# Kernel tuning notes

Hardware: AMD Instinct MI355X
Metric: run time of the kernel (lower is better)

## Reference

```python
import jax, jax.numpy as jnp
import numpy as np

B, BS, M, D = 64, 8, 512, 256  # b = bs * neg_sample_num, neg_sample_num = 8
NEG_FILL = -1e10


def setup_inputs() -> dict:
    key = jax.random.key(0)
    ks = jax.random.split(key, 7)
    x = jax.random.normal(ks[0], (B, M, D), jnp.float32)
    y = jax.random.normal(ks[1], (BS, M, D), jnp.float32)
    mask_x = jax.random.randint(ks[2], (B, M), 0, 2).astype(bool).at[:, 0].set(True)
    mask_y = jax.random.randint(ks[3], (BS, M), 0, 2).astype(bool).at[:, 0].set(True)
    scale = 1.0 / np.sqrt(D)
    Wq = jax.random.normal(ks[4], (D, D), jnp.float32) * scale  # torch Linear weight [out,in]
    Wk = jax.random.normal(ks[5], (D, D), jnp.float32) * scale
    Wv = jax.random.normal(ks[6], (D, D), jnp.float32) * scale
    return {"x": x, "y": y, "mask_x": mask_x, "mask_y": mask_y, "Wq": Wq, "Wk": Wk, "Wv": Wv}


def reference(x, y, mask_x, mask_y, Wq, Wk, Wv):
    # Projections (torch Linear: x @ W.T, no bias)
    Qx, Kx, Vx = x @ Wq.T, x @ Wk.T, x @ Wv.T
    Qy, Ky, Vy = y @ Wq.T, y @ Wk.T, y @ Wv.T
    b, m, d = Qx.shape
    bs = Ky.shape[0]
    neg = b // bs  # neg_sample_num branch (bs != b)

    scores_x = jnp.einsum('bid,bjd->bij', Qx, Kx)   # [b,m,m]
    scores_y = jnp.einsum('bid,bjd->bij', Qy, Ky)   # [bs,m,m]
    # Q_x grouped as [bs, neg, m, d] then transposed to [neg, bs, m, d];
    # K_y is tiled over neg (pure broadcast), so contract directly against [bs,m,d].
    Qx_e = Qx.reshape(bs, neg, m, d).swapaxes(0, 1)  # [neg,bs,m,d]
    scores_xy = jnp.einsum('nsid,sjd->nsij', Qx_e, Ky)  # [neg,bs,m,m]

    mx = mask_x[:, :, None]  # [b,m,1]
    my = mask_y[:, :, None]  # [bs,m,1]
    scores_x = jnp.where(mx & mx.swapaxes(1, 2), scores_x, NEG_FILL)
    scores_y = jnp.where(my & my.swapaxes(1, 2), scores_y, NEG_FILL)

    mask_xy = mask_x.reshape(bs, neg, m, 1).swapaxes(0, 1) & mask_y[None, :, None, :]  # [neg,bs,m,m]
    scores_xy = jnp.where(mask_xy, scores_xy, NEG_FILL)

    # y_len[n, s] = sum(mask_y[s]) for every n (repeat/view/sum/transpose in torch)
    y_len = jnp.broadcast_to(jnp.sum(mask_y.astype(jnp.int32), axis=1)[None, :], (neg, bs))

    probs_x = jax.nn.softmax(scores_x, axis=-1)
    probs_y = jax.nn.softmax(scores_y, axis=-1)
    probs_xy = jax.nn.softmax(scores_xy, axis=-1)

    ctx_x = jnp.einsum('bij,bjd->bid', probs_x, Vx)
    ctx_y = jnp.einsum('bij,bjd->bid', probs_y, Vy)
    return (ctx_x, ctx_y, scores_x, scores_y, probs_xy, mask_xy, y_len)
```

## Files before the change

### kernel.cpp

```cpp
#include <hip/hip_runtime.h>
#include <cstdint>

#define NEG_FILL_F (-10000000000.0f)
constexpr int BB     = 64;
constexpr int BS_    = 8;
constexpr int MM     = 512;
constexpr int DD     = 256;
constexpr int ROWS_X = BB * MM;
constexpr int ROWS_Y = BS_ * MM;
constexpr int ROWS_ALL = ROWS_X + ROWS_Y;
constexpr int KS     = 512;

typedef __attribute__((ext_vector_type(8))) short short8;
typedef __attribute__((ext_vector_type(4))) float f32x4;

__device__ inline unsigned short rne_bf16(float f) {
    unsigned int u = __float_as_uint(f);
    u = (u + 0x7FFFu + ((u >> 16) & 1u)) >> 16;
    return (unsigned short)u;
}
__device__ inline float bf2f(unsigned short h) {
    return __uint_as_float(((unsigned int)h) << 16);
}

__device__ inline f32x4 mfma16(short8 a, short8 b, f32x4 c) {
    return __builtin_amdgcn_mfma_f32_16x16x32_bf16(a, b, c, 0, 0, 0);
}

__device__ inline void gld16(const unsigned short* g, unsigned short* l) {
    __builtin_amdgcn_global_load_lds(
        (const __attribute__((address_space(1))) unsigned int*)g,
        (__attribute__((address_space(3))) unsigned int*)l, 16, 0, 0);
}

__device__ inline void mfma_4x4(const short8 af[4], const short8 bf_[4],
                                f32x4 acc[4][4]) {
    #pragma unroll
    for (int i = 0; i < 4; ++i)
        #pragma unroll
        for (int j = 0; j < 4; ++j)
            acc[i][j] = mfma16(af[i], bf_[j], acc[i][j]);
}

__device__ inline int awin(int w) { return ((((w >> 2) == 1) ? 256 : 0) + (w & 3) * 64); }
__device__ inline int bwin(int w) { return ((((w >> 2) == 2) ? 256 : 0) + (w & 3) * 64); }

__device__ inline void stage64(unsigned short* dstbase,
                               const unsigned short* __restrict__ src,
                               int srccol, int wave, int lane)
{
    #pragma unroll
    for (int s4 = 0; s4 < 4; ++s4) {
        const int c   = s4 * 256 + wave * 64 + lane;
        const int r   = c >> 3;
        const int cin = (c & 7) ^ (r & 7);
        gld16(src + (size_t)r * KS + srccol + cin * 8,
              dstbase + (size_t)(s4 * 256 + wave * 64) * 8);
    }
}

__device__ inline void frag4_x64(const unsigned short (*T)[64], int rbase,
                                 int lid, int c0, short8 f[4])
{
    const int q = c0 ^ (lid & 7);
    #pragma unroll
    for (int i = 0; i < 4; ++i)
        f[i] = *(const short8*)&T[rbase + i * 16 + lid][q * 8];
}

__global__ __launch_bounds__(256) void convw_kernel(
    const float* __restrict__ Wq, const float* __restrict__ Wk,
    const float* __restrict__ Wv, unsigned short* __restrict__ Wb)
{
    const int g  = blockIdx.x * 256 + threadIdx.x;
    const int e  = g * 8;
    const int zi = e >> 16;
    const int off = e & 65535;
    const int row = off >> 8, k0 = off & 255;
    const float* W = (zi == 0) ? Wq : (zi == 1 ? Wk : Wv);
    float4 v0 = *(const float4*)(W + off);
    float4 v1 = *(const float4*)(W + off + 4);
    const float fv[8] = {v0.x, v0.y, v0.z, v0.w, v1.x, v1.y, v1.z, v1.w};
    short8 hh, ll;
    #pragma unroll
    for (int i = 0; i < 8; ++i) {
        unsigned short h = rne_bf16(fv[i]);
        hh[i] = (short)h;
        ll[i] = (short)rne_bf16(fv[i] - bf2f(h));
    }
    unsigned short* dst = Wb + (size_t)zi * 131072 + (size_t)row * KS;
    *(short8*)(dst + k0)       = hh;
    *(short8*)(dst + 256 + k0) = ll;
}

__global__ __launch_bounds__(256) void convx_kernel(
    const float* __restrict__ x, const float* __restrict__ y,
    unsigned short* __restrict__ xs)
{
    const int g   = blockIdx.x * 256 + threadIdx.x;
    const int row = g >> 5;
    const int off = (g & 31) * 8;
    const float* src = (row < ROWS_X) ? (x + (size_t)row * DD)
                                      : (y + (size_t)(row - ROWS_X) * DD);
    float4 v0 = *(const float4*)(src + off);
    float4 v1 = *(const float4*)(src + off + 4);
    const float fv[8] = {v0.x, v0.y, v0.z, v0.w, v1.x, v1.y, v1.z, v1.w};
    short8 hh, ll;
    #pragma unroll
    for (int i = 0; i < 8; ++i) {
        unsigned short h = rne_bf16(fv[i]);
        hh[i] = (short)h;
        ll[i] = (short)rne_bf16(fv[i] - bf2f(h));
    }
    unsigned short* dst = xs + (size_t)row * KS;
    *(short8*)(dst + off)       = hh;
    *(short8*)(dst + 256 + off) = ll;
}

__global__ __launch_bounds__(256) void proj_kernel(
    const unsigned short* __restrict__ xs,
    const unsigned short* __restrict__ Wb,
    unsigned short* __restrict__ Qa, unsigned short* __restrict__ Kb,
    unsigned short* __restrict__ Vt)
{
    const int z    = blockIdx.z;
    const int row0 = blockIdx.x * 128;
    const int col0 = blockIdx.y * 128;
    const unsigned short* Asrc = xs + (size_t)row0 * KS;
    const unsigned short* Bsrc = Wb + (size_t)z * 131072 + (size_t)col0 * KS;

    __shared__ unsigned short Ab[128][64];
    __shared__ unsigned short Bb[128][64];

    const int t = threadIdx.x;
    const int wave = t >> 6, lane = t & 63, quad = lane >> 4, lid = lane & 15;
    const int wrow = (wave & 1) * 64, wcol = (wave >> 1) * 64;

    f32x4 acc[4][4];
    #pragma unroll
    for (int i = 0; i < 4; ++i)
        #pragma unroll
        for (int j = 0; j < 4; ++j) acc[i][j] = (f32x4){0.f, 0.f, 0.f, 0.f};

    for (int w = 0; w < 12; ++w) {
        stage64(&Ab[0][0], Asrc, awin(w), wave, lane);
        stage64(&Bb[0][0], Bsrc, bwin(w), wave, lane);
        __syncthreads();
        #pragma unroll
        for (int kk = 0; kk < 64; kk += 32) {
            const int c0 = (kk >> 3) + quad;
            short8 af[4], bf_[4];
            frag4_x64(Ab, wrow, lid, c0, af);
            frag4_x64(Bb, wcol, lid, c0, bf_);
            mfma_4x4(af, bf_, acc);
        }
        __syncthreads();
    }

    if (z == 2) {
        #pragma unroll
        for (int i = 0; i < 4; ++i) {
            const int rg = row0 + wrow + i * 16 + quad * 4;
            const int b  = rg >> 9;
            const int j  = rg & 511;
            #pragma unroll
            for (int jt = 0; jt < 4; ++jt) {
                const int col = col0 + wcol + jt * 16 + lid;
                *(ushort4*)(Vt + (size_t)b * DD * MM + (size_t)col * MM + j) =
                    make_ushort4(rne_bf16(acc[i][jt][0]), rne_bf16(acc[i][jt][1]),
                                 rne_bf16(acc[i][jt][2]), rne_bf16(acc[i][jt][3]));
            }
        }
    } else {
        unsigned short* dst = (z == 0) ? Qa : Kb;
        #pragma unroll
        for (int i = 0; i < 4; ++i) {
            const int rg = row0 + wrow + i * 16 + quad * 4;
            #pragma unroll
            for (int r = 0; r < 4; ++r) {
                unsigned short* rowp = dst + (size_t)(rg + r) * KS;
                #pragma unroll
                for (int jt = 0; jt < 4; ++jt) {
                    const int col = col0 + wcol + jt * 16 + lid;
                    const float v = acc[i][jt][r];
                    unsigned short h = rne_bf16(v);
                    rowp[col]       = h;
                    rowp[256 + col] = rne_bf16(v - bf2f(h));
                }
            }
        }
    }
}

__global__ __launch_bounds__(256) void scores_self_kernel(
    const unsigned short* __restrict__ Qa,
    const unsigned short* __restrict__ Kb,
    const int* __restrict__ mask_x, const int* __restrict__ mask_y,
    float* __restrict__ Sbase, float2* __restrict__ pstats)
{
    const int z    = blockIdx.z;
    const int row0 = blockIdx.x * 128;
    const int col0 = blockIdx.y * 128;
    const unsigned short* Asrc = Qa + (size_t)(z * MM + row0) * KS;
    const unsigned short* Bsrc = Kb + (size_t)(z * MM + col0) * KS;
    const int* msk = (z < 64) ? (mask_x + z * MM) : (mask_y + (z - 64) * MM);
    float* S = Sbase + (size_t)z * MM * MM;

    __shared__ unsigned short Ab[128][64];
    __shared__ unsigned short Bb[128][64];
    __shared__ float pm2[128][2];
    __shared__ float ps2[128][2];

    const int t = threadIdx.x;
    const int wave = t >> 6, lane = t & 63, quad = lane >> 4, lid = lane & 15;
    const int wrow = (wave & 1) * 64, wcol = (wave >> 1) * 64;

    f32x4 acc[4][4];
    #pragma unroll
    for (int i = 0; i < 4; ++i)
        #pragma unroll
        for (int j = 0; j < 4; ++j) acc[i][j] = (f32x4){0.f, 0.f, 0.f, 0.f};

    for (int w = 0; w < 12; ++w) {
        stage64(&Ab[0][0], Asrc, awin(w), wave, lane);
        stage64(&Bb[0][0], Bsrc, bwin(w), wave, lane);
        __syncthreads();
        #pragma unroll
        for (int kk = 0; kk < 64; kk += 32) {
            const int c0 = (kk >> 3) + quad;
            short8 af[4], bf_[4];
            frag4_x64(Ab, wrow, lid, c0, af);
            frag4_x64(Bb, wcol, lid, c0, bf_);
            mfma_4x4(af, bf_, acc);
        }
        __syncthreads();
    }

    int mcol[4];
    #pragma unroll
    for (int jt = 0; jt < 4; ++jt) mcol[jt] = msk[col0 + wcol + jt * 16 + lid];

    #pragma unroll
    for (int i = 0; i < 4; ++i) {
        const int rl0 = wrow + i * 16 + quad * 4;
        #pragma unroll
        for (int r = 0; r < 4; ++r) {
            const int rlocal = rl0 + r;
            const int rg = row0 + rlocal;
            const bool mr = (msk[rg] != 0);
            float* Srow = S + (size_t)rg * MM;
            float v[4];
            float mt = -3.4e38f;
            #pragma unroll
            for (int jt = 0; jt < 4; ++jt) {
                const int col = col0 + wcol + jt * 16 + lid;
                const bool valid = mr && (mcol[jt] != 0);
                v[jt] = valid ? acc[i][jt][r] : NEG_FILL_F;
                Srow[col] = v[jt];
                mt = fmaxf(mt, v[jt]);
            }
            #pragma unroll
            for (int o = 1; o < 16; o <<= 1) mt = fmaxf(mt, __shfl_xor(mt, o));
            float se = 0.f;
            #pragma unroll
            for (int jt = 0; jt < 4; ++jt) se += __expf(v[jt] - mt);
            #pragma unroll
            for (int o = 1; o < 16; o <<= 1) se += __shfl_xor(se, o);
            if (lid == 0) { pm2[rlocal][wave >> 1] = mt; ps2[rlocal][wave >> 1] = se; }
        }
    }
    __syncthreads();
    if (t < 128) {
        const float m0 = pm2[t][0], m1 = pm2[t][1];
        const float mm = fmaxf(m0, m1);
        const float ss = ps2[t][0] * __expf(m0 - mm) + ps2[t][1] * __expf(m1 - mm);
        pstats[(size_t)(z * 4 + blockIdx.y) * MM + row0 + t] = make_float2(mm, ss);
    }
}

__global__ __launch_bounds__(256) void scores_xy_kernel(
    const unsigned short* __restrict__ Qa, const unsigned short* __restrict__ Kb,
    const int* __restrict__ mask_x, const int* __restrict__ mask_y,
    float* __restrict__ Sbase, float* __restrict__ Mbase,
    float2* __restrict__ pstats)
{
    const int z = blockIdx.z;
    const int n = z >> 3, s = z & 7;
    const int bq = s * 8 + n;
    const int bk = s;
    const int row0 = blockIdx.x * 128;
    const int col0 = blockIdx.y * 128;
    const unsigned short* Asrc = Qa + (size_t)(bq * MM + row0) * KS;
    const unsigned short* Bsrc = Kb + (size_t)((ROWS_X + bk * MM) + col0) * KS;
    const int* mq = mask_x + bq * MM;
    const int* mk = mask_y + bk * MM;
    float* Sl = Sbase + (size_t)z * MM * MM;
    float* Ml = Mbase + (size_t)z * MM * MM;

    __shared__ unsigned short Ab[128][64];
    __shared__ unsigned short Bb[128][64];
    __shared__ float pm2[128][2];
    __shared__ float ps2[128][2];

    const int t = threadIdx.x;
    const int wave = t >> 6, lane = t & 63, quad = lane >> 4, lid = lane & 15;
    const int wrow = (wave & 1) * 64, wcol = (wave >> 1) * 64;

    f32x4 acc[4][4];
    #pragma unroll
    for (int i = 0; i < 4; ++i)
        #pragma unroll
        for (int j = 0; j < 4; ++j) acc[i][j] = (f32x4){0.f, 0.f, 0.f, 0.f};

    for (int ck = 0; ck < 4; ++ck) {
        stage64(&Ab[0][0], Asrc, ck * 64, wave, lane);
        stage64(&Bb[0][0], Bsrc, ck * 64, wave, lane);
        __syncthreads();
        #pragma unroll
        for (int kk = 0; kk < 64; kk += 32) {
            const int c0 = (kk >> 3) + quad;
            short8 af[4], bf_[4];
            frag4_x64(Ab, wrow, lid, c0, af);
            frag4_x64(Bb, wcol, lid, c0, bf_);
            mfma_4x4(af, bf_, acc);
        }
        __syncthreads();
    }

    int mcol[4];
    #pragma unroll
    for (int jt = 0; jt < 4; ++jt) mcol[jt] = mk[col0 + wcol + jt * 16 + lid];

    #pragma unroll
    for (int i = 0; i < 4; ++i) {
        const int rl0 = wrow + i * 16 + quad * 4;
        #pragma unroll
        for (int r = 0; r < 4; ++r) {
            const int rlocal = rl0 + r;
            const int rg = row0 + rlocal;
            const bool mr = (mq[rg] != 0);
            float* Srow = Sl + (size_t)rg * MM;
            float* Mrow = Ml + (size_t)rg * MM;
            float v[4];
            float mt = -3.4e38f;
            #pragma unroll
            for (int jt = 0; jt < 4; ++jt) {
                const int col = col0 + wcol + jt * 16 + lid;
                const bool valid = mr && (mcol[jt] != 0);
                v[jt] = valid ? acc[i][jt][r] : NEG_FILL_F;
                Srow[col] = v[jt];
                Mrow[col] = valid ? 1.0f : 0.0f;
                mt = fmaxf(mt, v[jt]);
            }
            #pragma unroll
            for (int o = 1; o < 16; o <<= 1) mt = fmaxf(mt, __shfl_xor(mt, o));
            float se = 0.f;
            #pragma unroll
            for (int jt = 0; jt < 4; ++jt) se += __expf(v[jt] - mt);
            #pragma unroll
            for (int o = 1; o < 16; o <<= 1) se += __shfl_xor(se, o);
            if (lid == 0) { pm2[rlocal][wave >> 1] = mt; ps2[rlocal][wave >> 1] = se; }
        }
    }
    __syncthreads();
    if (t < 128) {
        const float m0 = pm2[t][0], m1 = pm2[t][1];
        const float mm = fmaxf(m0, m1);
        const float ss = ps2[t][0] * __expf(m0 - mm) + ps2[t][1] * __expf(m1 - mm);
        pstats[(size_t)(z * 4 + blockIdx.y) * MM + row0 + t] = make_float2(mm, ss);
    }
}

__global__ __launch_bounds__(256) void reduce4_kernel(
    const float2* __restrict__ p, float2* __restrict__ st)
{
    const int row = blockIdx.x * 256 + threadIdx.x;
    const int z = row >> 9, rl = row & 511;
    float m = -3.4e38f, s = 0.f;
    #pragma unroll
    for (int by = 0; by < 4; ++by) {
        float2 v = p[(size_t)(z * 4 + by) * MM + rl];
        float nm = fmaxf(m, v.x);
        s = s * __expf(m - nm) + v.y * __expf(v.x - nm);
        m = nm;
    }
    st[row] = make_float2(m, 1.0f / s);
}

__global__ __launch_bounds__(256) void ctx_kernel(
    const float* __restrict__ Sbase, const float2* __restrict__ stats,
    const unsigned short* __restrict__ Vt_base, float* __restrict__ Obase)
{
    const int b = blockIdx.z;
    const float*          S  = Sbase + (size_t)b * MM * MM;
    const float2*         st = stats + (size_t)b * MM;
    const unsigned short* Vt = Vt_base + (size_t)b * DD * MM;
    float*                O  = Obase + (size_t)b * MM * DD;

    const int row0 = blockIdx.x * 128;
    const int col0 = blockIdx.y * 128;

    __shared__ unsigned short Ab[128][64];
    __shared__ unsigned short Bb[128][64];

    const int t = threadIdx.x;
    const int wave = t >> 6, lane = t & 63, quad = lane >> 4, lid = lane & 15;
    const int wrow = (wave & 1) * 64, wcol = (wave >> 1) * 64;

    f32x4 acc[4][4];
    #pragma unroll
    for (int i = 0; i < 4; ++i)
        #pragma unroll
        for (int j = 0; j < 4; ++j) acc[i][j] = (f32x4){0.f, 0.f, 0.f, 0.f};

    for (int ck = 0; ck < 8; ++ck) {
        #pragma unroll
        for (int s4 = 0; s4 < 4; ++s4) {
            const int c   = s4 * 256 + wave * 64 + lane;
            const int r   = c >> 3;
            const int cin = (c & 7) ^ (r & 7);
            gld16(Vt + (size_t)(col0 + r) * MM + ck * 64 + cin * 8,
                  &Bb[0][0] + (size_t)(s4 * 256 + wave * 64) * 8);
        }
        #pragma unroll
        for (int s4 = 0; s4 < 4; ++s4) {
            const int c    = s4 * 256 + t;
            const int row  = c >> 3;
            const int j8   = (c & 7) * 8;
            const int slot = (c & 7) ^ (row & 7);
            const float* sp = S + (size_t)(row0 + row) * MM + ck * 64 + j8;
            float4 v0 = *(const float4*)sp;
            float4 v1 = *(const float4*)(sp + 4);
            const float pm = st[row0 + row].x;
            short8 pk;
            pk[0] = (short)rne_bf16(__expf(v0.x - pm));
            pk[1] = (short)rne_bf16(__expf(v0.y - pm));
            pk[2] = (short)rne_bf16(__expf(v0.z - pm));
            pk[3] = (short)rne_bf16(__expf(v0.w - pm));
            pk[4] = (short)rne_bf16(__expf(v1.x - pm));
            pk[5] = (short)rne_bf16(__expf(v1.y - pm));
            pk[6] = (short)rne_bf16(__expf(v1.z - pm));
            pk[7] = (short)rne_bf16(__expf(v1.w - pm));
            *(short8*)&Ab[row][slot * 8] = pk;
        }
        __syncthreads();
        #pragma unroll
        for (int kk = 0; kk < 64; kk += 32) {
            const int c0 = (kk >> 3) + quad;
            short8 af[4], bf_[4];
            frag4_x64(Ab, wrow, lid, c0, af);
            frag4_x64(Bb, wcol, lid, c0, bf_);
            mfma_4x4(af, bf_, acc);
        }
        __syncthreads();
    }

    #pragma unroll
    for (int i = 0; i < 4; ++i) {
        const int rgb = row0 + wrow + i * 16 + quad * 4;
        float inv[4];
        #pragma unroll
        for (int r = 0; r < 4; ++r) inv[r] = st[rgb + r].y;
        #pragma unroll
        for (int jt = 0; jt < 4; ++jt) {
            const int col = col0 + wcol + jt * 16 + lid;
            #pragma unroll
            for (int r = 0; r < 4; ++r)
                O[(size_t)(rgb + r) * DD + col] = acc[i][jt][r] * inv[r];
        }
    }
}

__global__ __launch_bounds__(128) void softmax_apply(
    float* __restrict__ S, const float2* __restrict__ stats)
{
    const int row = blockIdx.x;
    const float2 st = stats[row];
    float4* r = (float4*)(S + (size_t)row * MM) + threadIdx.x;
    float4 v = *r;
    v.x = __expf(v.x - st.x) * st.y;
    v.y = __expf(v.y - st.x) * st.y;
    v.z = __expf(v.z - st.x) * st.y;
    v.w = __expf(v.w - st.x) * st.y;
    *r = v;
}

__global__ void ylen_kernel(const int* __restrict__ mask_y, float* __restrict__ out)
{
    const int s = blockIdx.x;
    const int lane = threadIdx.x;
    int c = 0;
    #pragma unroll
    for (int k = 0; k < 8; ++k) c += (mask_y[s * MM + k * 64 + lane] != 0);
    #pragma unroll
    for (int off = 32; off; off >>= 1) c += __shfl_xor(c, off);
    if (lane < 8) out[lane * 8 + s] = (float)c;
}

extern "C" void kernel_launch(void* const* d_in, const int* in_sizes, int n_in,
                              void* d_out, int out_size, void* d_ws, size_t ws_size,
                              hipStream_t stream)
{
    const float* x      = (const float*)d_in[0];
    const float* y      = (const float*)d_in[1];
    const int*   mask_x = (const int*)d_in[2];
    const int*   mask_y = (const int*)d_in[3];
    const float* Wq     = (const float*)d_in[4];
    const float* Wk     = (const float*)d_in[5];
    const float* Wv     = (const float*)d_in[6];
    float* out = (float*)d_out;

    unsigned short* Wb = (unsigned short*)d_ws;
    unsigned short* xs = Wb + 393216;
    unsigned short* Qa = xs + 18874368;
    unsigned short* Kb = Qa + 18874368;
    unsigned short* Vt = Kb + 18874368;
    float2* stats_x  = (float2*)(Vt + 9437184);
    float2* stats_xy = stats_x + ROWS_ALL;
    float2* ps_x  = stats_x + (ROWS_ALL + ROWS_X);
    float2* ps_xy = ps_x + (64 + 8) * 4 * 512;

    float* out_ctx_x = out;
    float* out_sx    = out + 9437184;
    float* out_pxy   = out + 28311552;
    float* out_mxy   = out + 45088768;
    float* out_ylen  = out + 61865984;

    convw_kernel<<<96, 256, 0, stream>>>(Wq, Wk, Wv, Wb);
    convx_kernel<<<4608, 256, 0, stream>>>(x, y, xs);
    ylen_kernel<<<8, 64, 0, stream>>>(mask_y, out_ylen);

    proj_kernel<<<dim3(288, 2, 3), 256, 0, stream>>>(xs, Wb, Qa, Kb, Vt);

    scores_self_kernel<<<dim3(4, 4, 72), 256, 0, stream>>>(
        Qa, Kb, mask_x, mask_y, out_sx, ps_x);
    scores_xy_kernel<<<dim3(4, 4, 64), 256, 0, stream>>>(
        Qa, Kb, mask_x, mask_y, out_pxy, out_mxy, ps_xy);

    reduce4_kernel<<<(ROWS_ALL + ROWS_X) / 256, 256, 0, stream>>>(ps_x, stats_x);

    softmax_apply<<<ROWS_X, 128, 0, stream>>>(out_pxy, stats_xy);

    ctx_kernel<<<dim3(4, 2, 72), 256, 0, stream>>>(out_sx, stats_x, Vt, out_ctx_x);
}
```

Before: 516.8 us.

## Double-buffer GEMM staging, add XCD-aware block remap, fuse xy stats reduction

Every GEMM kernel now stages K in 32-wide chunks into two LDS buffers, so the next chunk loads while the current one is multiplied, with one barrier per step. The grids are flattened and blocks are remapped so neighbouring tiles land on the same XCD, which should improve L2 reuse. The ctx kernel moves to 512 threads covering all 256 output columns, so the exp of S is computed once per row tile instead of twice. The xy partial-stats reduction is folded into softmax_apply, removing that part of reduce4. The cost is smaller K steps and more loop iterations, plus higher register and LDS pressure.

Result: faster. 485.2 us (-6.1%).

```diff
diff --git a/kernel.cpp b/kernel.cpp
--- a/kernel.cpp
+++ b/kernel.cpp
@@ -42,27 +42,27 @@
             acc[i][j] = mfma16(af[i], bf_[j], acc[i][j]);
 }
 
-__device__ inline int awin(int w) { return ((((w >> 2) == 1) ? 256 : 0) + (w & 3) * 64); }
-__device__ inline int bwin(int w) { return ((((w >> 2) == 2) ? 256 : 0) + (w & 3) * 64); }
-
-__device__ inline void stage64(unsigned short* dstbase,
+__device__ inline int awin32(int w) { return (((w >> 3) == 1) ? 256 : 0) + (w & 7) * 32; }
+__device__ inline int bwin32(int w) { return (((w >> 3) == 2) ? 256 : 0) + (w & 7) * 32; }
+
+__device__ inline void stage32(unsigned short* dstbase,
                                const unsigned short* __restrict__ src,
                                int srccol, int wave, int lane)
 {
     #pragma unroll
-    for (int s4 = 0; s4 < 4; ++s4) {
+    for (int s4 = 0; s4 < 2; ++s4) {
         const int c   = s4 * 256 + wave * 64 + lane;
-        const int r   = c >> 3;
-        const int cin = (c & 7) ^ (r & 7);
+        const int r   = c >> 2;
+        const int cin = (c & 3) ^ (r & 3);
         gld16(src + (size_t)r * KS + srccol + cin * 8,
               dstbase + (size_t)(s4 * 256 + wave * 64) * 8);
     }
 }
 
-__device__ inline void frag4_x64(const unsigned short (*T)[64], int rbase,
-                                 int lid, int c0, short8 f[4])
-{
-    const int q = c0 ^ (lid & 7);
+__device__ inline void frag4_x32(const unsigned short (*T)[32], int rbase,
+                                 int lid, int quad, short8 f[4])
+{
+    const int q = quad ^ (lid & 3);
     #pragma unroll
     for (int i = 0; i < 4; ++i)
         f[i] = *(const short8*)&T[rbase + i * 16 + lid][q * 8];
@@ -123,14 +123,18 @@
     unsigned short* __restrict__ Qa, unsigned short* __restrict__ Kb,
     unsigned short* __restrict__ Vt)
 {
-    const int z    = blockIdx.z;
-    const int row0 = blockIdx.x * 128;
-    const int col0 = blockIdx.y * 128;
+    const int xcd = blockIdx.x & 7, idx = blockIdx.x >> 3;
+    const int lin = xcd * 216 + idx;
+    const int bx  = lin / 6;
+    const int rem = lin - bx * 6;
+    const int z    = rem >> 1;
+    const int row0 = bx * 128;
+    const int col0 = (rem & 1) * 128;
     const unsigned short* Asrc = xs + (size_t)row0 * KS;
     const unsigned short* Bsrc = Wb + (size_t)z * 131072 + (size_t)col0 * KS;
 
-    __shared__ unsigned short Ab[128][64];
-    __shared__ unsigned short Bb[128][64];
+    __shared__ unsigned short Ab[2][128][32];
+    __shared__ unsigned short Bb[2][128][32];
 
     const int t = threadIdx.x;
     const int wave = t >> 6, lane = t & 63, quad = lane >> 4, lid = lane & 15;
@@ -142,19 +146,25 @@
         #pragma unroll
         for (int j = 0; j < 4; ++j) acc[i][j] = (f32x4){0.f, 0.f, 0.f, 0.f};
 
-    for (int w = 0; w < 12; ++w) {
-        stage64(&Ab[0][0], Asrc, awin(w), wave, lane);
-        stage64(&Bb[0][0], Bsrc, bwin(w), wave, lane);
+    stage32(&Ab[0][0][0], Asrc, awin32(0), wave, lane);
+    stage32(&Bb[0][0][0], Bsrc, bwin32(0), wave, lane);
+    __syncthreads();
+    int cur = 0;
+    for (int w = 0; w < 23; ++w) {
+        stage32(&Ab[cur ^ 1][0][0], Asrc, awin32(w + 1), wave, lane);
+        stage32(&Bb[cur ^ 1][0][0], Bsrc, bwin32(w + 1), wave, lane);
+        short8 af[4], bf_[4];
+        frag4_x32(Ab[cur], wrow, lid, quad, af);
+        frag4_x32(Bb[cur], wcol, lid, quad, bf_);
+        mfma_4x4(af, bf_, acc);
         __syncthreads();
-        #pragma unroll
-        for (int kk = 0; kk < 64; kk += 32) {
-            const int c0 = (kk >> 3) + quad;
-            short8 af[4], bf_[4];
-            frag4_x64(Ab, wrow, lid, c0, af);
-            frag4_x64(Bb, wcol, lid, c0, bf_);
-            mfma_4x4(af, bf_, acc);
-        }
-        __syncthreads();
+        cur ^= 1;
+    }
+    {
+        short8 af[4], bf_[4];
+        frag4_x32(Ab[cur], wrow, lid, quad, af);
+        frag4_x32(Bb[cur], wcol, lid, quad, bf_);
+        mfma_4x4(af, bf_, acc);
     }
 
     if (z == 2) {
@@ -198,16 +208,20 @@
     const int* __restrict__ mask_x, const int* __restrict__ mask_y,
     float* __restrict__ Sbase, float2* __restrict__ pstats)
 {
-    const int z    = blockIdx.z;
-    const int row0 = blockIdx.x * 128;
-    const int col0 = blockIdx.y * 128;
+    const int xcd = blockIdx.x & 7, idx = blockIdx.x >> 3;
+    const int lin = xcd * 144 + idx;
+    const int z   = lin >> 4;
+    const int rem = lin & 15;
+    const int row0 = (rem & 3) * 128;
+    const int col0 = (rem >> 2) * 128;
+    const int by   = rem >> 2;
     const unsigned short* Asrc = Qa + (size_t)(z * MM + row0) * KS;
     const unsigned short* Bsrc = Kb + (size_t)(z * MM + col0) * KS;
     const int* msk = (z < 64) ? (mask_x + z * MM) : (mask_y + (z - 64) * MM);
     float* S = Sbase + (size_t)z * MM * MM;
 
-    __shared__ unsigned short Ab[128][64];
-    __shared__ unsigned short Bb[128][64];
+    __shared__ unsigned short Ab[2][128][32];
+    __shared__ unsigned short Bb[2][128][32];
     __shared__ float pm2[128][2];
     __shared__ float ps2[128][2];
 
@@ -221,19 +235,25 @@
         #pragma unroll
         for (int j = 0; j < 4; ++j) acc[i][j] = (f32x4){0.f, 0.f, 0.f, 0.f};
 
-    for (int w = 0; w < 12; ++w) {
-        stage64(&Ab[0][0], Asrc, awin(w), wave, lane);
-        stage64(&Bb[0][0], Bsrc, bwin(w), wave, lane);
+    stage32(&Ab[0][0][0], Asrc, awin32(0), wave, lane);
+    stage32(&Bb[0][0][0], Bsrc, bwin32(0), wave, lane);
+    __syncthreads();
+    int cur = 0;
+    for (int w = 0; w < 23; ++w) {
+        stage32(&Ab[cur ^ 1][0][0], Asrc, awin32(w + 1), wave, lane);
+        stage32(&Bb[cur ^ 1][0][0], Bsrc, bwin32(w + 1), wave, lane);
+        short8 af[4], bf_[4];
+        frag4_x32(Ab[cur], wrow, lid, quad, af);
+        frag4_x32(Bb[cur], wcol, lid, quad, bf_);
+        mfma_4x4(af, bf_, acc);
         __syncthreads();
-        #pragma unroll
-        for (int kk = 0; kk < 64; kk += 32) {
-            const int c0 = (kk >> 3) + quad;
-            short8 af[4], bf_[4];
-            frag4_x64(Ab, wrow, lid, c0, af);
-            frag4_x64(Bb, wcol, lid, c0, bf_);
-            mfma_4x4(af, bf_, acc);
-        }
-        __syncthreads();
+        cur ^= 1;
+    }
+    {
+        short8 af[4], bf_[4];
+        frag4_x32(Ab[cur], wrow, lid, quad, af);
+        frag4_x32(Bb[cur], wcol, lid, quad, bf_);
+        mfma_4x4(af, bf_, acc);
     }
 
     int mcol[4];
@@ -274,7 +294,7 @@
         const float m0 = pm2[t][0], m1 = pm2[t][1];
         const float mm = fmaxf(m0, m1);
         const float ss = ps2[t][0] * __expf(m0 - mm) + ps2[t][1] * __expf(m1 - mm);
-        pstats[(size_t)(z * 4 + blockIdx.y) * MM + row0 + t] = make_float2(mm, ss);
+        pstats[(size_t)(z * 4 + by) * MM + row0 + t] = make_float2(mm, ss);
     }
 }
 
@@ -284,21 +304,26 @@
     float* __restrict__ Sbase, float* __restrict__ Mbase,
     float2* __restrict__ pstats)
 {
-    const int z = blockIdx.z;
-    const int n = z >> 3, s = z & 7;
+    const int xcd = blockIdx.x & 7, idx = blockIdx.x >> 3;
+    const int lin = xcd * 128 + idx;
+    const int zz  = lin >> 4;
+    const int rem = lin & 15;
+    const int s = zz >> 3, n = zz & 7;
+    const int zo = n * 8 + s;
     const int bq = s * 8 + n;
     const int bk = s;
-    const int row0 = blockIdx.x * 128;
-    const int col0 = blockIdx.y * 128;
+    const int row0 = (rem & 3) * 128;
+    const int col0 = (rem >> 2) * 128;
+    const int by   = rem >> 2;
     const unsigned short* Asrc = Qa + (size_t)(bq * MM + row0) * KS;
     const unsigned short* Bsrc = Kb + (size_t)((ROWS_X + bk * MM) + col0) * KS;
     const int* mq = mask_x + bq * MM;
     const int* mk = mask_y + bk * MM;
-    float* Sl = Sbase + (size_t)z * MM * MM;
-    float* Ml = Mbase + (size_t)z * MM * MM;
-
-    __shared__ unsigned short Ab[128][64];
-    __shared__ unsigned short Bb[128][64];
+    float* Sl = Sbase + (size_t)zo * MM * MM;
+    float* Ml = Mbase + (size_t)zo * MM * MM;
+
+    __shared__ unsigned short Ab[2][128][32];
+    __shared__ unsigned short Bb[2][128][32];
     __shared__ float pm2[128][2];
     __shared__ float ps2[128][2];
 
@@ -312,19 +337,25 @@
         #pragma unroll
         for (int j = 0; j < 4; ++j) acc[i][j] = (f32x4){0.f, 0.f, 0.f, 0.f};
 
-    for (int ck = 0; ck < 4; ++ck) {
-        stage64(&Ab[0][0], Asrc, ck * 64, wave, lane);
-        stage64(&Bb[0][0], Bsrc, ck * 64, wave, lane);
+    stage32(&Ab[0][0][0], Asrc, 0, wave, lane);
+    stage32(&Bb[0][0][0], Bsrc, 0, wave, lane);
+    __syncthreads();
+    int cur = 0;
+    for (int w = 0; w < 7; ++w) {
+        stage32(&Ab[cur ^ 1][0][0], Asrc, (w + 1) * 32, wave, lane);
+        stage32(&Bb[cur ^ 1][0][0], Bsrc, (w + 1) * 32, wave, lane);
+        short8 af[4], bf_[4];
+        frag4_x32(Ab[cur], wrow, lid, quad, af);
+        frag4_x32(Bb[cur], wcol, lid, quad, bf_);
+        mfma_4x4(af, bf_, acc);
         __syncthreads();
-        #pragma unroll
-        for (int kk = 0; kk < 64; kk += 32) {
-            const int c0 = (kk >> 3) + quad;
-            short8 af[4], bf_[4];
-            frag4_x64(Ab, wrow, lid, c0, af);
-            frag4_x64(Bb, wcol, lid, c0, bf_);
-            mfma_4x4(af, bf_, acc);
-        }
-        __syncthreads();
+        cur ^= 1;
+    }
+    {
+        short8 af[4], bf_[4];
+        frag4_x32(Ab[cur], wrow, lid, quad, af);
+        frag4_x32(Bb[cur], wcol, lid, quad, bf_);
+        mfma_4x4(af, bf_, acc);
     }
 
     int mcol[4];
@@ -367,7 +398,7 @@
         const float m0 = pm2[t][0], m1 = pm2[t][1];
         const float mm = fmaxf(m0, m1);
         const float ss = ps2[t][0] * __expf(m0 - mm) + ps2[t][1] * __expf(m1 - mm);
-        pstats[(size_t)(z * 4 + blockIdx.y) * MM + row0 + t] = make_float2(mm, ss);
+        pstats[(size_t)(zo * 4 + by) * MM + row0 + t] = make_float2(mm, ss);
     }
 }
 
@@ -387,21 +418,21 @@
     st[row] = make_float2(m, 1.0f / s);
 }
 
-__global__ __launch_bounds__(256) void ctx_kernel(
+__global__ __launch_bounds__(512) void ctx_kernel(
     const float* __restrict__ Sbase, const float2* __restrict__ stats,
     const unsigned short* __restrict__ Vt_base, float* __restrict__ Obase)
 {
-    const int b = blockIdx.z;
+    const int xcd = blockIdx.x & 7, idx = blockIdx.x >> 3;
+    const int lin = xcd * 36 + idx;
+    const int b    = lin >> 2;
+    const int row0 = (lin & 3) * 128;
     const float*          S  = Sbase + (size_t)b * MM * MM;
     const float2*         st = stats + (size_t)b * MM;
     const unsigned short* Vt = Vt_base + (size_t)b * DD * MM;
     float*                O  = Obase + (size_t)b * MM * DD;
 
-    const int row0 = blockIdx.x * 128;
-    const int col0 = blockIdx.y * 128;
-
-    __shared__ unsigned short Ab[128][64];
-    __shared__ unsigned short Bb[128][64];
+    __shared__ unsigned short Abuf[2][128][32];
+    __shared__ unsigned short Bbuf[2][256][32];
 
     const int t = threadIdx.x;
     const int wave = t >> 6, lane = t & 63, quad = lane >> 4, lid = lane & 15;
@@ -413,46 +444,56 @@
         #pragma unroll
         for (int j = 0; j < 4; ++j) acc[i][j] = (f32x4){0.f, 0.f, 0.f, 0.f};
 
-    for (int ck = 0; ck < 8; ++ck) {
-        #pragma unroll
-        for (int s4 = 0; s4 < 4; ++s4) {
-            const int c   = s4 * 256 + wave * 64 + lane;
-            const int r   = c >> 3;
-            const int cin = (c & 7) ^ (r & 7);
-            gld16(Vt + (size_t)(col0 + r) * MM + ck * 64 + cin * 8,
-                  &Bb[0][0] + (size_t)(s4 * 256 + wave * 64) * 8);
+    auto stageB = [&](unsigned short* dstbase, int w) {
+        #pragma unroll
+        for (int s4 = 0; s4 < 2; ++s4) {
+            const int c   = s4 * 512 + wave * 64 + lane;
+            const int r   = c >> 2;
+            const int cin = (c & 3) ^ (r & 3);
+            gld16(Vt + (size_t)r * MM + w * 32 + cin * 8,
+                  dstbase + (size_t)(s4 * 512 + wave * 64) * 8);
         }
-        #pragma unroll
-        for (int s4 = 0; s4 < 4; ++s4) {
-            const int c    = s4 * 256 + t;
-            const int row  = c >> 3;
-            const int j8   = (c & 7) * 8;
-            const int slot = (c & 7) ^ (row & 7);
-            const float* sp = S + (size_t)(row0 + row) * MM + ck * 64 + j8;
-            float4 v0 = *(const float4*)sp;
-            float4 v1 = *(const float4*)(sp + 4);
-            const float pm = st[row0 + row].x;
-            short8 pk;
-            pk[0] = (short)rne_bf16(__expf(v0.x - pm));
-            pk[1] = (short)rne_bf16(__expf(v0.y - pm));
-            pk[2] = (short)rne_bf16(__expf(v0.z - pm));
-            pk[3] = (short)rne_bf16(__expf(v0.w - pm));
-            pk[4] = (short)rne_bf16(__expf(v1.x - pm));
-            pk[5] = (short)rne_bf16(__expf(v1.y - pm));
-            pk[6] = (short)rne_bf16(__expf(v1.z - pm));
-            pk[7] = (short)rne_bf16(__expf(v1.w - pm));
-            *(short8*)&Ab[row][slot * 8] = pk;
-        }
+    };
+    auto stageA = [&](unsigned short (*Ab)[32], int w) {
+        const int c    = t;
+        const int r    = c >> 2;
+        const int q    = c & 3;
+        const int slot = q ^ (r & 3);
+        const float* sp = S + (size_t)(row0 + r) * MM + w * 32 + q * 8;
+        float4 v0 = *(const float4*)sp;
+        float4 v1 = *(const float4*)(sp + 4);
+        const float pm = st[row0 + r].x;
+        short8 pk;
+        pk[0] = (short)rne_bf16(__expf(v0.x - pm));
+        pk[1] = (short)rne_bf16(__expf(v0.y - pm));
+        pk[2] = (short)rne_bf16(__expf(v0.z - pm));
+        pk[3] = (short)rne_bf16(__expf(v0.w - pm));
+        pk[4] = (short)rne_bf16(__expf(v1.x - pm));
+        pk[5] = (short)rne_bf16(__expf(v1.y - pm));
+        pk[6] = (short)rne_bf16(__expf(v1.z - pm));
+        pk[7] = (short)rne_bf16(__expf(v1.w - pm));
+        *(short8*)&Ab[r][slot * 8] = pk;
+    };
+
+    stageB(&Bbuf[0][0][0], 0);
+    stageA(Abuf[0], 0);
+    __syncthreads();
+    int cur = 0;
+    for (int w = 0; w < 15; ++w) {
+        stageB(&Bbuf[cur ^ 1][0][0], w + 1);
+        stageA(Abuf[cur ^ 1], w + 1);
+        short8 af[4], bf_[4];
+        frag4_x32(Abuf[cur], wrow, lid, quad, af);
+        frag4_x32(Bbuf[cur], wcol, lid, quad, bf_);
+        mfma_4x4(af, bf_, acc);
         __syncthreads();
-        #pragma unroll
-        for (int kk = 0; kk < 64; kk += 32) {
-            const int c0 = (kk >> 3) + quad;
-            short8 af[4], bf_[4];
-            frag4_x64(Ab, wrow, lid, c0, af);
-            frag4_x64(Bb, wcol, lid, c0, bf_);
-            mfma_4x4(af, bf_, acc);
-        }
-        __syncthreads();
+        cur ^= 1;
+    }
+    {
+        short8 af[4], bf_[4];
+        frag4_x32(Abuf[cur], wrow, lid, quad, af);
+        frag4_x32(Bbuf[cur], wcol, lid, quad, bf_);
+        mfma_4x4(af, bf_, acc);
     }
 
     #pragma unroll
@@ -463,7 +504,7 @@
         for (int r = 0; r < 4; ++r) inv[r] = st[rgb + r].y;
         #pragma unroll
         for (int jt = 0; jt < 4; ++jt) {
-            const int col = col0 + wcol + jt * 16 + lid;
+            const int col = wcol + jt * 16 + lid;
             #pragma unroll
             for (int r = 0; r < 4; ++r)
                 O[(size_t)(rgb + r) * DD + col] = acc[i][jt][r] * inv[r];
@@ -472,16 +513,25 @@
 }
 
 __global__ __launch_bounds__(128) void softmax_apply(
-    float* __restrict__ S, const float2* __restrict__ stats)
+    float* __restrict__ S, const float2* __restrict__ ps)
 {
     const int row = blockIdx.x;
-    const float2 st = stats[row];
+    const int z = row >> 9, rl = row & 511;
+    float m = -3.4e38f, s = 0.f;
+    #pragma unroll
+    for (int by = 0; by < 4; ++by) {
+        float2 v = ps[(size_t)(z * 4 + by) * MM + rl];
+        float nm = fmaxf(m, v.x);
+        s = s * __expf(m - nm) + v.y * __expf(v.x - nm);
+        m = nm;
+    }
+    const float inv = 1.0f / s;
     float4* r = (float4*)(S + (size_t)row * MM) + threadIdx.x;
     float4 v = *r;
-    v.x = __expf(v.x - st.x) * st.y;
-    v.y = __expf(v.y - st.x) * st.y;
-    v.z = __expf(v.z - st.x) * st.y;
-    v.w = __expf(v.w - st.x) * st.y;
+    v.x = __expf(v.x - m) * inv;
+    v.y = __expf(v.y - m) * inv;
+    v.z = __expf(v.z - m) * inv;
+    v.w = __expf(v.w - m) * inv;
     *r = v;
 }
 
@@ -515,10 +565,9 @@
     unsigned short* Qa = xs + 18874368;
     unsigned short* Kb = Qa + 18874368;
     unsigned short* Vt = Kb + 18874368;
-    float2* stats_x  = (float2*)(Vt + 9437184);
-    float2* stats_xy = stats_x + ROWS_ALL;
-    float2* ps_x  = stats_x + (ROWS_ALL + ROWS_X);
-    float2* ps_xy = ps_x + (64 + 8) * 4 * 512;
+    float2* stats_x = (float2*)(Vt + 9437184);
+    float2* ps_x    = stats_x + ROWS_ALL;
+    float2* ps_xy   = ps_x + 72 * 4 * 512;
 
     float* out_ctx_x = out;
     float* out_sx    = out + 9437184;
@@ -530,16 +579,16 @@
     convx_kernel<<<4608, 256, 0, stream>>>(x, y, xs);
     ylen_kernel<<<8, 64, 0, stream>>>(mask_y, out_ylen);
 
-    proj_kernel<<<dim3(288, 2, 3), 256, 0, stream>>>(xs, Wb, Qa, Kb, Vt);
-
-    scores_self_kernel<<<dim3(4, 4, 72), 256, 0, stream>>>(
+    proj_kernel<<<1728, 256, 0, stream>>>(xs, Wb, Qa, Kb, Vt);
+
+    scores_self_kernel<<<1152, 256, 0, stream>>>(
         Qa, Kb, mask_x, mask_y, out_sx, ps_x);
-    scores_xy_kernel<<<dim3(4, 4, 64), 256, 0, stream>>>(
+    scores_xy_kernel<<<1024, 256, 0, stream>>>(
         Qa, Kb, mask_x, mask_y, out_pxy, out_mxy, ps_xy);
 
-    reduce4_kernel<<<(ROWS_ALL + ROWS_X) / 256, 256, 0, stream>>>(ps_x, stats_x);
-
-    softmax_apply<<<ROWS_X, 128, 0, stream>>>(out_pxy, stats_xy);
-
-    ctx_kernel<<<dim3(4, 2, 72), 256, 0, stream>>>(out_sx, stats_x, Vt, out_ctx_x);
-}
+    reduce4_kernel<<<ROWS_ALL / 256, 256, 0, stream>>>(ps_x, stats_x);
+
+    softmax_apply<<<ROWS_X, 128, 0, stream>>>(out_pxy, ps_xy);
+
+    ctx_kernel<<<288, 512, 0, stream>>>(out_sx, stats_x, Vt, out_ctx_x);
+}
```
